# Kernel tuning notes

Hardware: AMD Instinct MI355X
Metric: run time of the kernel (lower is better)

Reference implementation:

```python
import jax, jax.numpy as jnp
import numpy as np

OUT, IN = 4096, 4096
GROUP = 128
N_GROUPS = IN // GROUP  # 32, remainder_cols == 0
BITS_PRIMARY = 4
BITS_RESIDUAL = 2
EPS = 1e-12


def setup_inputs() -> dict:
    key = jax.random.key(0)
    ks = jax.random.split(key, 6)
    return {
        "x": jax.random.normal(ks[0], (4, 2048, IN), dtype=jnp.float32),
        "norms_primary": jax.random.uniform(ks[1], (OUT, N_GROUPS), dtype=jnp.float32),
        "norms_residual": jax.random.uniform(ks[2], (OUT, N_GROUPS), dtype=jnp.float32),
        "bias": jax.random.normal(ks[3], (OUT,), dtype=jnp.float32),
        "idx_primary": jax.random.randint(ks[4], (OUT, N_GROUPS, GROUP), 0, 2 ** BITS_PRIMARY, dtype=jnp.int32),
        "idx_residual": jax.random.randint(ks[5], (OUT, N_GROUPS, GROUP), 0, 2 ** BITS_RESIDUAL, dtype=jnp.int32),
    }


def _dequant(idx, norms, bits):
    # Codebook: symmetric uniform levels in [-1, 1]; TurboQuant stores a
    # unit-direction per group (codes) plus its L2 norm (fp32 scale).
    levels = jnp.linspace(-1.0, 1.0, 2 ** bits, dtype=norms.dtype)
    q = levels[idx]                                             # [O, G, gs]
    unit = q * jax.lax.rsqrt(jnp.sum(q * q, axis=-1, keepdims=True) + EPS)
    w = norms[..., None] * unit                                 # [O, G, gs]
    return w.reshape(w.shape[0], -1)                            # [O, IN]


def reference(x, norms_primary, norms_residual, bias, idx_primary, idx_residual):
    # primary reconstruction + residual correction, then dense matmul
    w = _dequant(idx_primary, norms_primary, BITS_PRIMARY) \
        + _dequant(idx_residual, norms_residual, BITS_RESIDUAL)  # [OUT, IN]
    w = w.astype(x.dtype)
    # F.linear: y = x @ W^T + b
    return jnp.einsum('bsi,oi->bso', x, w) + bias.astype(x.dtype)
```

## Files before the change

### kernel.cpp

```cpp
#include <hip/hip_runtime.h>
#include <hip/hip_bf16.h>
#include <stdint.h>

#define OUT_DIM 4096
#define IN_DIM  4096
#define GROUPSZ 128
#define NGROUPS 32
#define M_TOTAL 8192
#define EPS_Q   1e-12f

#define BM 256
#define BN 256
#define BK 32
#define NT (IN_DIM / BK)

typedef float f32x4   __attribute__((ext_vector_type(4)));
typedef float float4v __attribute__((ext_vector_type(4)));
typedef short bf16x8  __attribute__((ext_vector_type(8)));

static __device__ __forceinline__ short f2bf(float f) {
    union { float f; unsigned u; } v; v.f = f;
    unsigned r = v.u + 0x7fffu + ((v.u >> 16) & 1u);
    return (short)(r >> 16);
}

#define GLOAD16(gp, lp) __builtin_amdgcn_global_load_lds( \
    (const __attribute__((address_space(1))) void*)(gp),  \
    (__attribute__((address_space(3))) void*)(lp), 16, 0, 0)

__global__ __launch_bounds__(256) void dequant_kernel(
    const float* __restrict__ norms_p, const float* __restrict__ norms_r,
    const int* __restrict__ idx_p, const int* __restrict__ idx_r,
    short* __restrict__ W)
{
    const int gid  = (int)((blockIdx.x * 256u + threadIdx.x) >> 6);
    const int lane = threadIdx.x & 63;
    const size_t base = (size_t)gid * GROUPSZ;

    const int ip0 = idx_p[base + lane];
    const int ip1 = idx_p[base + lane + 64];
    const int ir0 = idx_r[base + lane];
    const int ir1 = idx_r[base + lane + 64];

    const float qp0 = -1.f + (2.f / 15.f) * (float)ip0;
    const float qp1 = -1.f + (2.f / 15.f) * (float)ip1;
    const float qr0 = -1.f + (2.f / 3.f)  * (float)ir0;
    const float qr1 = -1.f + (2.f / 3.f)  * (float)ir1;

    float ssp = qp0 * qp0 + qp1 * qp1;
    float ssr = qr0 * qr0 + qr1 * qr1;
    #pragma unroll
    for (int m = 32; m >= 1; m >>= 1) {
        ssp += __shfl_xor(ssp, m);
        ssr += __shfl_xor(ssr, m);
    }
    const float sp = norms_p[gid] / sqrtf(ssp + EPS_Q);
    const float sr = norms_r[gid] / sqrtf(ssr + EPS_Q);

    W[base + lane]      = f2bf(qp0 * sp + qr0 * sr);
    W[base + lane + 64] = f2bf(qp1 * sp + qr1 * sr);
}

__global__ __launch_bounds__(256) void cast_kernel(
    const float* __restrict__ x, short* __restrict__ xb)
{
    const size_t i = ((size_t)blockIdx.x * 256u + threadIdx.x) * 8u;
    float4v a = *(const float4v*)(x + i);
    float4v b = *(const float4v*)(x + i + 4);
    bf16x8 o;
    o[0] = f2bf(a[0]); o[1] = f2bf(a[1]); o[2] = f2bf(a[2]); o[3] = f2bf(a[3]);
    o[4] = f2bf(b[0]); o[5] = f2bf(b[1]); o[6] = f2bf(b[2]); o[7] = f2bf(b[3]);
    *(bf16x8*)(xb + i) = o;
}

__global__ __launch_bounds__(512, 2) void gemm_kernel(
    const short* __restrict__ A,
    const short* __restrict__ B,
    const float* __restrict__ bias,
    float* __restrict__ C)
{
    __shared__ short lds[65536];

    const int tid  = threadIdx.x;
    const int lane = tid & 63;
    const int wid  = tid >> 6;
    const int wr   = wid >> 2;
    const int wc   = wid & 3;

    const int nwg = gridDim.x;
    const int cpx = nwg >> 3;
    const int wg  = ((int)blockIdx.x & 7) * cpx + ((int)blockIdx.x >> 3);
    const int ntile = wg & 15;
    const int mtile = wg >> 4;
    const size_t brow = (size_t)mtile * BM;
    const size_t bcol = (size_t)ntile * BN;

    const int s0 = tid, s1 = tid + 512;
    const int r0 = s0 >> 2, c0 = (s0 & 3) ^ ((r0 >> 1) & 3);
    const int r1 = s1 >> 2, c1 = (s1 & 3) ^ ((r1 >> 1) & 3);

    const short* aG0 = A + (brow + (size_t)r0) * IN_DIM + c0 * 8;
    const short* aG1 = A + (brow + (size_t)r1) * IN_DIM + c1 * 8;
    const short* bG0 = B + (bcol + (size_t)r0) * IN_DIM + c0 * 8;
    const short* bG1 = B + (bcol + (size_t)r1) * IN_DIM + c1 * 8;

    short* ldA0 = lds + s0 * 8;
    short* ldA1 = lds + s1 * 8;
    short* ldB0 = lds + 32768 + s0 * 8;
    short* ldB1 = lds + 32768 + s1 * 8;

    const int fr   = lane & 15;
    const int kc   = lane >> 4;
    const int xorc = kc ^ ((fr >> 1) & 3);
    const int aBase = wr * 4096 + fr * 32 + xorc * 8;
    const int bBase = 32768 + wc * 2048 + fr * 32 + xorc * 8;

    f32x4 acc[8][4] = {};

    auto stage = [&](int t) {
        const int boff = (t & 3) * 8192;
        const int ko   = t * BK;
        GLOAD16(aG0 + ko, ldA0 + boff);
        GLOAD16(aG1 + ko, ldA1 + boff);
        GLOAD16(bG0 + ko, ldB0 + boff);
        GLOAD16(bG1 + ko, ldB1 + boff);
    };

    auto compute = [&](int t) {
        const short* pA = lds + (t & 3) * 8192 + aBase;
        const short* pB = lds + (t & 3) * 8192 + bBase;
        bf16x8 af[8], bf[4];
        #pragma unroll
        for (int m = 0; m < 8; ++m) af[m] = *(const bf16x8*)(pA + m * 512);
        #pragma unroll
        for (int n = 0; n < 4; ++n) bf[n] = *(const bf16x8*)(pB + n * 512);
        __builtin_amdgcn_s_setprio(1);
        #pragma unroll
        for (int m = 0; m < 8; ++m)
            #pragma unroll
            for (int n = 0; n < 4; ++n)
                acc[m][n] = __builtin_amdgcn_mfma_f32_16x16x32_bf16(
                    af[m], bf[n], acc[m][n], 0, 0, 0);
        __builtin_amdgcn_s_setprio(0);
    };

    stage(0); stage(1); stage(2);

    #pragma unroll 1
    for (int t = 0; t < NT - 3; ++t) {
        asm volatile("s_waitcnt vmcnt(8)" ::: "memory");
        __builtin_amdgcn_s_barrier();
        __builtin_amdgcn_sched_barrier(0);
        stage(t + 3);
        compute(t);
    }
    asm volatile("s_waitcnt vmcnt(8)" ::: "memory");
    __builtin_amdgcn_s_barrier();
    __builtin_amdgcn_sched_barrier(0);
    compute(NT - 3);
    asm volatile("s_waitcnt vmcnt(4)" ::: "memory");
    __builtin_amdgcn_s_barrier();
    __builtin_amdgcn_sched_barrier(0);
    compute(NT - 2);
    asm volatile("s_waitcnt vmcnt(0)" ::: "memory");
    __builtin_amdgcn_s_barrier();
    __builtin_amdgcn_sched_barrier(0);
    compute(NT - 1);

    #pragma unroll
    for (int n = 0; n < 4; ++n) {
        const int col = (int)bcol + wc * 64 + n * 16 + fr;
        const float bv = bias[col];
        #pragma unroll
        for (int m = 0; m < 8; ++m) {
            const size_t row0 = brow + wr * 128 + m * 16 + kc * 4;
            #pragma unroll
            for (int r = 0; r < 4; ++r)
                C[(row0 + r) * OUT_DIM + col] = acc[m][n][r] + bv;
        }
    }
}

extern "C" void kernel_launch(void* const* d_in, const int* in_sizes, int n_in,
                              void* d_out, int out_size, void* d_ws, size_t ws_size,
                              hipStream_t stream)
{
    const float* x        = (const float*)d_in[0];
    const float* norms_p  = (const float*)d_in[1];
    const float* norms_r  = (const float*)d_in[2];
    const float* bias     = (const float*)d_in[3];
    const int*   idx_p    = (const int*)d_in[4];
    const int*   idx_r    = (const int*)d_in[5];
    float*       out      = (float*)d_out;

    short* xb = (short*)d_ws;
    short* wq = (short*)d_ws + (size_t)M_TOTAL * IN_DIM;

    dequant_kernel<<<(OUT_DIM * NGROUPS) / 4, 256, 0, stream>>>(
        norms_p, norms_r, idx_p, idx_r, wq);

    cast_kernel<<<(int)(((size_t)M_TOTAL * IN_DIM) / (256 * 8)), 256, 0, stream>>>(x, xb);

    gemm_kernel<<<(M_TOTAL / BM) * (OUT_DIM / BN), 512, 0, stream>>>(xb, wq, bias, out);
}
```

Before: 303.3 us.

## Restructure GEMM mainloop into BK=64 quadrant-pipelined double-buffered schedule

The GEMM main loop moves from a 4-deep BK=32 ring buffer to a double-buffered BK=64 tile. Each tile is split into four half-A/half-B quadrants whose global-to-LDS loads are interleaved with MFMA blocks, separated by explicit barriers and waitcnts. The warp-to-output mapping changes to 2x2 sub-quadrants and the LDS swizzle becomes an 8-way XOR. The goal is to overlap loads with compute at finer grain and halve loop iterations, at the cost of many more barriers per tile and tricky vmcnt accounting.

Measured after the change: 292.8 us. -3.5%, faster.

```diff
diff --git a/kernel.cpp b/kernel.cpp
--- a/kernel.cpp
+++ b/kernel.cpp
@@ -11,7 +11,7 @@
 
 #define BM 256
 #define BN 256
-#define BK 32
+#define BK 64
 #define NT (IN_DIM / BK)
 
 typedef float f32x4   __attribute__((ext_vector_type(4)));
@@ -73,9 +73,46 @@
     *(bf16x8*)(xb + i) = o;
 }
 
+template<int HA, int HB>
+__device__ __forceinline__ void mfma_quad(f32x4 (&acc)[2][2][4][2],
+                                          const bf16x8 (&af)[4][2],
+                                          const bf16x8 (&bf)[2][2]) {
+#pragma unroll
+    for (int m = 0; m < 4; ++m)
+#pragma unroll
+        for (int n = 0; n < 2; ++n)
+#pragma unroll
+            for (int kh = 0; kh < 2; ++kh)
+                acc[HA][HB][m][n] = __builtin_amdgcn_mfma_f32_16x16x32_bf16(
+                    af[m][kh], bf[n][kh], acc[HA][HB][m][n], 0, 0, 0);
+}
+
+static __device__ __forceinline__ void rd8(const short* base, int ck0, int ck1,
+                                           bf16x8 (&f)[4][2]) {
+#pragma unroll
+    for (int m = 0; m < 4; ++m) {
+        f[m][0] = *(const bf16x8*)(base + m * 1024 + ck0);
+        f[m][1] = *(const bf16x8*)(base + m * 1024 + ck1);
+    }
+}
+
+static __device__ __forceinline__ void rd4(const short* base, int ck0, int ck1,
+                                           bf16x8 (&f)[2][2]) {
+#pragma unroll
+    for (int n = 0; n < 2; ++n) {
+        f[n][0] = *(const bf16x8*)(base + n * 1024 + ck0);
+        f[n][1] = *(const bf16x8*)(base + n * 1024 + ck1);
+    }
+}
+
+#define BARRIER()  asm volatile("s_barrier" ::: "memory")
+#define LGKM0()    do { asm volatile("s_waitcnt lgkmcnt(0)" ::: "memory"); \
+                        __builtin_amdgcn_sched_barrier(0); } while (0)
+#define WAITV(N)   asm volatile("s_waitcnt vmcnt(" #N ")" ::: "memory")
+
 __global__ __launch_bounds__(512, 2) void gemm_kernel(
-    const short* __restrict__ A,
-    const short* __restrict__ B,
+    const short* __restrict__ Ag,
+    const short* __restrict__ Bg,
     const float* __restrict__ bias,
     float* __restrict__ C)
 {
@@ -86,99 +123,104 @@
     const int wid  = tid >> 6;
     const int wr   = wid >> 2;
     const int wc   = wid & 3;
+    const int fr   = lane & 15;
+    const int lq   = lane >> 4;
 
     const int nwg = gridDim.x;
     const int cpx = nwg >> 3;
     const int wg  = ((int)blockIdx.x & 7) * cpx + ((int)blockIdx.x >> 3);
     const int ntile = wg & 15;
     const int mtile = wg >> 4;
-    const size_t brow = (size_t)mtile * BM;
-    const size_t bcol = (size_t)ntile * BN;
-
-    const int s0 = tid, s1 = tid + 512;
-    const int r0 = s0 >> 2, c0 = (s0 & 3) ^ ((r0 >> 1) & 3);
-    const int r1 = s1 >> 2, c1 = (s1 & 3) ^ ((r1 >> 1) & 3);
-
-    const short* aG0 = A + (brow + (size_t)r0) * IN_DIM + c0 * 8;
-    const short* aG1 = A + (brow + (size_t)r1) * IN_DIM + c1 * 8;
-    const short* bG0 = B + (bcol + (size_t)r0) * IN_DIM + c0 * 8;
-    const short* bG1 = B + (bcol + (size_t)r1) * IN_DIM + c1 * 8;
-
-    short* ldA0 = lds + s0 * 8;
-    short* ldA1 = lds + s1 * 8;
-    short* ldB0 = lds + 32768 + s0 * 8;
-    short* ldB1 = lds + 32768 + s1 * 8;
-
-    const int fr   = lane & 15;
-    const int kc   = lane >> 4;
-    const int xorc = kc ^ ((fr >> 1) & 3);
-    const int aBase = wr * 4096 + fr * 32 + xorc * 8;
-    const int bBase = 32768 + wc * 2048 + fr * 32 + xorc * 8;
-
-    f32x4 acc[8][4] = {};
-
-    auto stage = [&](int t) {
-        const int boff = (t & 3) * 8192;
-        const int ko   = t * BK;
-        GLOAD16(aG0 + ko, ldA0 + boff);
-        GLOAD16(aG1 + ko, ldA1 + boff);
-        GLOAD16(bG0 + ko, ldB0 + boff);
-        GLOAD16(bG1 + ko, ldB1 + boff);
+    const uint32_t brow = (uint32_t)mtile * BM;
+    const uint32_t bcol = (uint32_t)ntile * BN;
+
+    const uint32_t sr_ = (uint32_t)(tid >> 3);
+    const uint32_t gc_ = (uint32_t)((tid & 7) ^ ((tid >> 3) & 7));
+    const uint32_t aOffB = (brow + sr_) * IN_DIM + gc_ * 8;
+    const uint32_t bOffB = (bcol + sr_) * IN_DIM + gc_ * 8;
+
+    auto stage = [&](const short* M, uint32_t baseOff, uint32_t extra, short* dstRegion) {
+        GLOAD16(M + baseOff + extra,            dstRegion + tid * 8);
+        GLOAD16(M + baseOff + extra + 262144u,  dstRegion + tid * 8 + 4096);
     };
 
-    auto compute = [&](int t) {
-        const short* pA = lds + (t & 3) * 8192 + aBase;
-        const short* pB = lds + (t & 3) * 8192 + bBase;
-        bf16x8 af[8], bf[4];
-        #pragma unroll
-        for (int m = 0; m < 8; ++m) af[m] = *(const bf16x8*)(pA + m * 512);
-        #pragma unroll
-        for (int n = 0; n < 4; ++n) bf[n] = *(const bf16x8*)(pB + n * 512);
-        __builtin_amdgcn_s_setprio(1);
-        #pragma unroll
-        for (int m = 0; m < 8; ++m)
-            #pragma unroll
-            for (int n = 0; n < 4; ++n)
-                acc[m][n] = __builtin_amdgcn_mfma_f32_16x16x32_bf16(
-                    af[m], bf[n], acc[m][n], 0, 0, 0);
-        __builtin_amdgcn_s_setprio(0);
-    };
-
-    stage(0); stage(1); stage(2);
+    const int c0  = (lq ^ (fr & 7));
+    const int ck0 = c0 * 8;
+    const int ck1 = (c0 ^ 4) * 8;
+    const int aRd = (wr * 64 + fr) * 64;
+    const int bRd = (wc * 32 + fr) * 64;
+
+    f32x4  acc[2][2][4][2] = {};
+    bf16x8 af[4][2], bf0[2][2], bf1[2][2];
+
+    stage(Ag, aOffB, 0u,            lds);
+    stage(Bg, bOffB, 0u,            lds + 16384);
+    stage(Ag, aOffB, 524288u,       lds + 8192);
+    stage(Bg, bOffB, 524288u,       lds + 24576);
+    stage(Ag, aOffB, 64u,           lds + 32768);
+    stage(Bg, bOffB, 64u,           lds + 32768 + 16384);
+    WAITV(8);
+    BARRIER();
+
+#define TILE_BODY(T, STG0, STG1, STG2, STG3, WAIT_P0, WAIT_P3) do {           \
+    short* sb = lds + (((T) & 1) ? 32768 : 0);                                \
+    short* ob = lds + (((T) & 1) ? 0 : 32768);                                \
+                                                   \
+    rd8(sb + aRd, ck0, ck1, af);                                              \
+    rd4(sb + 16384 + bRd, ck0, ck1, bf0);                                     \
+    if (STG0) stage(Ag, aOffB, 524288u + (uint32_t)((T) + 1) * 64u, ob + 8192); \
+    BARRIER(); LGKM0();                                                       \
+    __builtin_amdgcn_s_setprio(1); mfma_quad<0,0>(acc, af, bf0);              \
+    __builtin_amdgcn_s_setprio(0);                                            \
+    WAIT_P0;                                                                  \
+    BARRIER();                                                                \
+                                                   \
+    rd4(sb + 24576 + bRd, ck0, ck1, bf1);                                     \
+    if (STG1) stage(Bg, bOffB, 524288u + (uint32_t)((T) + 1) * 64u, ob + 24576); \
+    BARRIER(); LGKM0();                                                       \
+    __builtin_amdgcn_s_setprio(1); mfma_quad<0,1>(acc, af, bf1);              \
+    __builtin_amdgcn_s_setprio(0);                                            \
+    BARRIER();                                                                \
+                                                   \
+    rd8(sb + 8192 + aRd, ck0, ck1, af);                                       \
+    if (STG2) stage(Ag, aOffB, (uint32_t)((T) + 2) * 64u, sb);                \
+    BARRIER(); LGKM0();                                                       \
+    __builtin_amdgcn_s_setprio(1); mfma_quad<1,0>(acc, af, bf0);              \
+    __builtin_amdgcn_s_setprio(0);                                            \
+    BARRIER();                                                                \
+                                                   \
+    if (STG3) stage(Bg, bOffB, (uint32_t)((T) + 2) * 64u, sb + 16384);        \
+    BARRIER(); LGKM0();                                                       \
+    __builtin_amdgcn_s_setprio(1); mfma_quad<1,1>(acc, af, bf1);              \
+    __builtin_amdgcn_s_setprio(0);                                            \
+    WAIT_P3;                                                                  \
+    BARRIER();                                                                \
+} while (0)
 
     #pragma unroll 1
-    for (int t = 0; t < NT - 3; ++t) {
-        asm volatile("s_waitcnt vmcnt(8)" ::: "memory");
-        __builtin_amdgcn_s_barrier();
-        __builtin_amdgcn_sched_barrier(0);
-        stage(t + 3);
-        compute(t);
-    }
-    asm volatile("s_waitcnt vmcnt(8)" ::: "memory");
-    __builtin_amdgcn_s_barrier();
-    __builtin_amdgcn_sched_barrier(0);
-    compute(NT - 3);
-    asm volatile("s_waitcnt vmcnt(4)" ::: "memory");
-    __builtin_amdgcn_s_barrier();
-    __builtin_amdgcn_sched_barrier(0);
-    compute(NT - 2);
-    asm volatile("s_waitcnt vmcnt(0)" ::: "memory");
-    __builtin_amdgcn_s_barrier();
-    __builtin_amdgcn_sched_barrier(0);
-    compute(NT - 1);
-
-    #pragma unroll
-    for (int n = 0; n < 4; ++n) {
-        const int col = (int)bcol + wc * 64 + n * 16 + fr;
+    for (int t = 0; t < NT - 2; ++t) {
+        TILE_BODY(t, 1, 1, 1, 1, WAITV(6), WAITV(8));
+    }
+    TILE_BODY(NT - 2, 1, 1, 0, 0, WAITV(6), WAITV(4));
+    TILE_BODY(NT - 1, 0, 0, 0, 0, WAITV(0), (void)0);
+
+    #pragma unroll
+    for (int hA = 0; hA < 2; ++hA)
+    #pragma unroll
+    for (int hB = 0; hB < 2; ++hB)
+    #pragma unroll
+    for (int n = 0; n < 2; ++n) {
+        const int col = (int)bcol + hB * 128 + wc * 32 + n * 16 + fr;
         const float bv = bias[col];
         #pragma unroll
-        for (int m = 0; m < 8; ++m) {
-            const size_t row0 = brow + wr * 128 + m * 16 + kc * 4;
+        for (int m = 0; m < 4; ++m) {
+            const size_t row0 = (size_t)brow + hA * 128 + wr * 64 + m * 16 + lq * 4;
             #pragma unroll
             for (int r = 0; r < 4; ++r)
-                C[(row0 + r) * OUT_DIM + col] = acc[m][n][r] + bv;
+                C[(row0 + r) * OUT_DIM + col] = acc[hA][hB][m][n][r] + bv;
         }
     }
+#undef TILE_BODY
 }
 
 extern "C" void kernel_launch(void* const* d_in, const int* in_sizes, int n_in,
```
